# Kernel optimization log

Hardware: AMD Instinct MI355X
Metric: run time of the kernel (lower is better)

The kernel has to match this reference:

```python
import jax, jax.numpy as jnp
import numpy as np

# --- low precision float format: exp=5, man=2, subnormals, nearest-even ---
EXP, MAN = 5, 2
BIAS = 2 ** (EXP - 1) - 1          # 15
EMIN = 1 - BIAS                     # -14 (min normal exponent; clamping here gives subnormals)
MAXV = (2.0 - 2.0 ** (-MAN)) * 2.0 ** BIAS


def _q(x):
    """Round x to nearest FP(exp=5, man=2) value (subnormals, clipped at max)."""
    ax = jnp.abs(x)
    e = jnp.floor(jnp.log2(jnp.where(ax > 0, ax, 1.0)))
    e = jnp.maximum(e, EMIN)
    scale = jnp.exp2(e - MAN)
    q = jnp.round(x / scale) * scale   # jnp.round = half-to-even
    q = jnp.clip(q, -MAXV, MAXV)
    return jnp.where(ax > 0, q, x).astype(x.dtype)


# Quantizer: forward quantize, straight-through (quantized) backward
@jax.custom_vjp
def fq(x):
    return _q(x)

def _fq_fwd(x):
    return _q(x), None

def _fq_bwd(_, g):
    return (_q(g),)

fq.defvjp(_fq_fwd, _fq_bwd)


def conv_valid(x, w):
    return jax.lax.conv_general_dilated(
        x, w, window_strides=(1, 1), padding='VALID',
        dimension_numbers=('NCHW', 'OIHW', 'NCHW'))


def qconv(x, w):
    # QConv2d: input_quant, weight_quant, conv, output_quant
    return fq(conv_valid(fq(x), fq(w)))


def qlinear(x, W, b):
    # QLinear: input_quant, weight_quant (weights + bias), matmul, output_quant
    return fq(fq(x) @ fq(W).T + fq(b))


def batchnorm(x, gamma, beta, eps=1e-5):
    # training-mode BatchNorm2d over (N,H,W) per channel
    m = x.mean(axis=(0, 2, 3), keepdims=True)
    v = x.var(axis=(0, 2, 3), keepdims=True)
    return (x - m) * jax.lax.rsqrt(v + eps) * gamma[None, :, None, None] + beta[None, :, None, None]


def maxpool2(x):
    return jax.lax.reduce_window(x, -jnp.inf, jax.lax.max,
                                 (1, 1, 2, 2), (1, 1, 2, 2), 'VALID')


def setup_inputs() -> dict:
    key = jax.random.key(0)
    ks = jax.random.split(key, 12)
    B = 8192
    inp = {
        'x':   jax.random.normal(ks[0], (B, 1, 32, 32), jnp.float32),
        'w1':  jax.random.normal(ks[1], (6, 1, 5, 5), jnp.float32) * 0.2,
        'g1':  jnp.ones((6,), jnp.float32),
        'be1': jnp.zeros((6,), jnp.float32),
        'w2':  jax.random.normal(ks[2], (16, 6, 5, 5), jnp.float32) * 0.1,
        'g2':  jnp.ones((16,), jnp.float32),
        'be2': jnp.zeros((16,), jnp.float32),
        'fw1': jax.random.normal(ks[3], (120, 400), jnp.float32) * 0.05,
        'fb1': jnp.zeros((120,), jnp.float32),
        'fw2': jax.random.normal(ks[4], (84, 120), jnp.float32) * 0.09,
        'fb2': jnp.zeros((84,), jnp.float32),
        'fw3': jax.random.normal(ks[5], (10, 84), jnp.float32) * 0.1,
        'fb3': jnp.zeros((10,), jnp.float32),
    }
    return inp


def reference(x, w1, g1, be1, w2, g2, be2, fw1, fb1, fw2, fb2, fw3, fb3):
    x = fq(x)                                   # act_error_quant
    x = qconv(x, w1)                            # conv1 (no bias)
    x = batchnorm(x, g1, be1)                   # bn1
    x = fq(x)                                   # act_error_quant
    x = maxpool2(jax.nn.relu(x))                # relu + 2x2 maxpool -> [B,6,14,14]
    x = qconv(x, w2)                            # conv2 -> [B,16,10,10]
    x = batchnorm(x, g2, be2)                   # bn2
    x = fq(x)
    x = maxpool2(jax.nn.relu(x))                # -> [B,16,5,5]
    x = x.reshape(x.shape[0], -1)               # [B,400]
    x = jax.nn.relu(qlinear(x, fw1, fb1))       # fc1
    x = jax.nn.relu(qlinear(x, fw2, fb2))       # fc2
    x = qlinear(x, fw3, fb3)                    # fc3 -> [B,10]
    return x
```

## Files before the change

### kernel.cpp

```cpp
#include <hip/hip_runtime.h>
#include <hip/hip_bf16.h>


#define BATCH 8192

typedef double d4 __attribute__((ext_vector_type(4)));

__device__ __forceinline__ double fq_d(double x) {
    long long b = __double_as_longlong(x);
    long long ab = b & 0x7fffffffffffffffLL;
    if (ab == 0) return x;
    double q;
    if (ab >= 0x3F10000000000000LL) {
        long long r = b + 0x0001FFFFFFFFFFFFLL + ((b >> 50) & 1LL);
        r &= 0xFFFC000000000000LL;
        q = __longlong_as_double(r);
        q = fmin(fmax(q, -57344.0), 57344.0);
    } else {
        q = rint(x * 65536.0) * 1.52587890625e-05;
    }
    return q;
}

__device__ __forceinline__ float fq_f(float x) {
    int b = __float_as_int(x);
    int ab = b & 0x7fffffff;
    if (ab == 0) return x;
    float q;
    if (ab >= 0x38800000) {
        int r = b + 0x000FFFFF + ((b >> 21) & 1);
        r &= 0xFFE00000;
        q = __int_as_float(r);
        q = fminf(fmaxf(q, -57344.0f), 57344.0f);
    } else {
        q = rintf(x * 65536.0f) * 1.52587890625e-05f;
    }
    return q;
}

__device__ __forceinline__ unsigned short bfbits(double q) {
    __hip_bfloat16 h = __float2bfloat16((float)q);
    return *(unsigned short*)&h;
}

__device__ __forceinline__ float bfval(unsigned short u) {
    return __bfloat162float(*(__hip_bfloat16*)&u);
}

__global__ void kprep(const float* __restrict__ w1, const float* __restrict__ w2,
                      const float* __restrict__ fb1, const float* __restrict__ fb2,
                      const float* __restrict__ fb3, const float* __restrict__ fw1,
                      const float* __restrict__ fw2, const float* __restrict__ fw3,
                      float* __restrict__ qw1, float* __restrict__ qw2t,
                      float* __restrict__ qfb1, float* __restrict__ qfb2,
                      float* __restrict__ qfb3, float* __restrict__ Wt1,
                      float* __restrict__ Wt2, float* __restrict__ Wt3) {
    int i = blockIdx.x * 256 + threadIdx.x;
    if (i < 150) { qw1[i] = fq_f(w1[i]); return; }
    i -= 150;
    if (i < 2432) { int k = i >> 4, co = i & 15;
        qw2t[i] = (k < 150) ? fq_f(w2[co * 150 + k]) : 0.0f; return; }
    i -= 2432;
    if (i < 120) { qfb1[i] = fq_f(fb1[i]); return; }
    i -= 120;
    if (i < 84) { qfb2[i] = fq_f(fb2[i]); return; }
    i -= 84;
    if (i < 10) { qfb3[i] = fq_f(fb3[i]); return; }
    i -= 10;
    if (i < 51200) { int k = i / 128, o = i % 128;
        Wt1[i] = (o < 120) ? fq_f(fw1[o * 400 + k]) : 0.0f; return; }
    i -= 51200;
    if (i < 15360) { int k = i / 128, o = i % 128;
        Wt2[i] = (o < 84) ? fq_f(fw2[o * 120 + k]) : 0.0f; return; }
    i -= 15360;
    if (i < 1344) { int k = i / 16, o = i % 16;
        Wt3[i] = (o < 10) ? fq_f(fw3[o * 84 + k]) : 0.0f; return; }
}
#define PREP_TOTAL (150 + 2432 + 120 + 84 + 10 + 51200 + 15360 + 1344)

__global__ __launch_bounds__(512) void kconv1(const float* __restrict__ x,
        const float* __restrict__ qw, const float* __restrict__ g1,
        unsigned short* __restrict__ praw, int nimg_total,
        double* __restrict__ st1) {
    __shared__ float sxf[3 * 1056];
    __shared__ double swd[152];
    __shared__ float sg1[6];
    __shared__ double sred[6][2];
    int t = threadIdx.x;
    int b0 = blockIdx.x * 3;
    int nimg = nimg_total - b0; if (nimg > 3) nimg = 3;
    for (int i = t; i < nimg * 1024; i += 512) {
        int img = i >> 10, idx = i & 1023;
        sxf[img * 1056 + (idx >> 5) * 33 + (idx & 31)] =
            fq_f(x[(size_t)(b0 + img) * 1024 + idx]);
    }
    if (t < 150) swd[t] = (double)qw[t];
    if (t >= 160 && t < 166) sg1[t - 160] = g1[t - 160];
    if (t >= 192 && t < 204) ((double*)sred)[t - 192] = 0.0;
    __syncthreads();
    int ntask = nimg * 168;
    for (int task = t; task < ntask; task += 512) {
        int img = task / 168; int rr = task % 168;
        int co = rr / 28; int rem = rr % 28;
        int ph = rem >> 1;
        int half = rem & 1;
        int i0 = 2 * ph;
        int j0 = half * 14;
        const double* wp = &swd[co * 25];
        double a0[14], a1[14];
        #pragma unroll
        for (int j = 0; j < 14; ++j) { a0[j] = 0.0; a1[j] = 0.0; }
        double wr[5], wq[5];
        #pragma unroll
        for (int u = 0; u < 6; ++u) {
            const float* xr = &sxf[img * 1056 + (i0 + u) * 33 + j0];
            double xv[18];
            #pragma unroll
            for (int k = 0; k < 18; ++k) xv[k] = (double)xr[k];
            if (u < 5) {
                #pragma unroll
                for (int tt = 0; tt < 5; ++tt) wr[tt] = wp[u * 5 + tt];
                #pragma unroll
                for (int j = 0; j < 14; ++j)
                    a0[j] = fma(xv[j], wr[0], fma(xv[j+1], wr[1], fma(xv[j+2], wr[2],
                            fma(xv[j+3], wr[3], fma(xv[j+4], wr[4], a0[j])))));
            }
            if (u >= 1) {
                #pragma unroll
                for (int j = 0; j < 14; ++j)
                    a1[j] = fma(xv[j], wq[0], fma(xv[j+1], wq[1], fma(xv[j+2], wq[2],
                            fma(xv[j+3], wq[3], fma(xv[j+4], wq[4], a1[j])))));
            }
            #pragma unroll
            for (int tt = 0; tt < 5; ++tt) wq[tt] = wr[tt];
        }
        double q0[14], q1[14];
        double s = 0.0, s2 = 0.0;
        #pragma unroll
        for (int j = 0; j < 14; ++j) {
            q0[j] = fq_d(a0[j]); q1[j] = fq_d(a1[j]);
            s += q0[j] + q1[j]; s2 += q0[j] * q0[j] + q1[j] * q1[j];
        }
        bool useMax = (sg1[co] >= 0.0f);
        unsigned short* dst = praw + ((size_t)(b0 + img) * 6 + co) * 196 + ph * 14 + half * 7;
        #pragma unroll
        for (int jp = 0; jp < 7; ++jp) {
            double pmax = fmax(fmax(q0[2*jp], q0[2*jp+1]), fmax(q1[2*jp], q1[2*jp+1]));
            double pmin = fmin(fmin(q0[2*jp], q0[2*jp+1]), fmin(q1[2*jp], q1[2*jp+1]));
            dst[jp] = bfbits(useMax ? pmax : pmin);
        }
        atomicAdd(&sred[co][0], s);
        atomicAdd(&sred[co][1], s2);
    }
    __syncthreads();
    if (t < 12) atomicAdd(&st1[t * 32 + (blockIdx.x & 31)], ((double*)sred)[t]);
}

__global__ void kfinal(const double* __restrict__ st, double* __restrict__ mr,
                       int C, double N) {
    int c = threadIdx.x;
    if (c < C) {
        double s = 0.0, s2 = 0.0;
        for (int b = 0; b < 32; ++b) { s += st[c * 64 + b]; s2 += st[c * 64 + 32 + b]; }
        double m = s / N;
        double v = s2 / N - m * m;
        mr[2 * c] = m;
        mr[2 * c + 1] = 1.0 / sqrt(v + 1e-5);
    }
}

__global__ __launch_bounds__(256) void kbn1(const unsigned short* __restrict__ praw,
        const double* __restrict__ mr1, const float* __restrict__ g1,
        const float* __restrict__ be1, __hip_bfloat16* __restrict__ p1) {
    int idx = blockIdx.x * 256 + threadIdx.x;
    int cb = idx / 49;
    int c = cb % 6;
    int off = (idx % 49) * 4;
    double m = mr1[2 * c], r = mr1[2 * c + 1];
    double gg = (double)g1[c], bb = (double)be1[c];
    ushort4 u = *(const ushort4*)(praw + (size_t)cb * 196 + off);
    ushort4 o;
    double q;
    q = fq_d((((double)bfval(u.x) - m) * r) * gg + bb); o.x = bfbits(fmax(q, 0.0));
    q = fq_d((((double)bfval(u.y) - m) * r) * gg + bb); o.y = bfbits(fmax(q, 0.0));
    q = fq_d((((double)bfval(u.z) - m) * r) * gg + bb); o.z = bfbits(fmax(q, 0.0));
    q = fq_d((((double)bfval(u.w) - m) * r) * gg + bb); o.w = bfbits(fmax(q, 0.0));
    *(ushort4*)((unsigned short*)p1 + (size_t)cb * 196 + off) = o;
}

__global__ __launch_bounds__(512) void kconv2(const __hip_bfloat16* __restrict__ p1,
        const float* __restrict__ qw2t, __hip_bfloat16* __restrict__ c2,
        double* __restrict__ st2) {
    __shared__ float sxf[9408];
    __shared__ float swf[2432];
    __shared__ int soff[152];
    __shared__ unsigned short sep[8][256];
    __shared__ double sred[16][2];
    int t = threadIdx.x;
    int b0 = blockIdx.x * 8;
    const ushort4* srcp = (const ushort4*)(p1 + (size_t)b0 * 1176);
    for (int i = t; i < 2352; i += 512) {
        ushort4 u = srcp[i];
        float* d = &sxf[4 * i];
        d[0] = bfval(u.x);
        d[1] = bfval(u.y);
        d[2] = bfval(u.z);
        d[3] = bfval(u.w);
    }
    {
        const float4* wsrc = (const float4*)qw2t;
        float4* wdst = (float4*)swf;
        for (int i = t; i < 608; i += 512) wdst[i] = wsrc[i];
    }
    if (t < 152)
        soff[t] = (t < 150) ? (t / 25) * 196 + ((t % 25) / 5) * 14 + (t % 5) : 0;
    if (t < 32) ((double*)sred)[t] = 0.0;
    __syncthreads();

    int l = t & 63, w = t >> 6;
    int c = l >> 4, r16 = l & 15;

    d4 pz = {0.0, 0.0, 0.0, 0.0};
    d4 prow = __builtin_amdgcn_mfma_f64_16x16x4f64((double)r16, 0.25, pz, 0, 0, 0);
    d4 pcol = __builtin_amdgcn_mfma_f64_16x16x4f64(1.0, 0.25 * (double)r16, pz, 0, 0, 0);
    int rowidx[4], colidx[4];
    #pragma unroll
    for (int j = 0; j < 4; ++j) { rowidx[j] = (int)prow[j]; colidx[j] = (int)pcol[j]; }

    unsigned short* myep = sep[w];
    double ls = 0.0, ls2 = 0.0;
    int co0 = colidx[0];
    for (int tile = w; tile < 50; tile += 8) {
        int pos = tile * 16 + r16;
        int abase = (pos / 100) * 1176 + ((pos % 100) / 10) * 14 + (pos % 10);
        d4 a0 = {0.0, 0.0, 0.0, 0.0}, a1 = {0.0, 0.0, 0.0, 0.0};
        #pragma unroll
        for (int s = 0; s < 19; ++s) {
            int k0 = 4 * s + c;
            int k1 = 4 * (s + 19) + c;
            double x0 = (double)sxf[abase + soff[k0]];
            double x1 = (double)sxf[abase + soff[k1]];
            double w0 = (double)swf[k0 * 16 + r16];
            double w1 = (double)swf[k1 * 16 + r16];
            a0 = __builtin_amdgcn_mfma_f64_16x16x4f64(x0, w0, a0, 0, 0, 0);
            a1 = __builtin_amdgcn_mfma_f64_16x16x4f64(x1, w1, a1, 0, 0, 0);
        }
        #pragma unroll
        for (int j = 0; j < 4; ++j) {
            double q = fq_d(a0[j] + a1[j]);
            myep[rowidx[j] * 16 + colidx[j]] = bfbits(q);
            ls += q; ls2 += q * q;
        }
        ushort4 v = *(const ushort4*)&myep[l * 4];
        *(ushort4*)((unsigned short*)c2 + ((size_t)b0 * 100 + tile * 16) * 16 + l * 4) = v;
    }
    atomicAdd(&sred[co0][0], ls);
    atomicAdd(&sred[co0][1], ls2);
    __syncthreads();
    if (t < 32) atomicAdd(&st2[t * 32 + (blockIdx.x & 31)], ((double*)sred)[t]);
}

__global__ __launch_bounds__(256) void kfc1(const __hip_bfloat16* __restrict__ c2,
        const double* __restrict__ st2, const float* __restrict__ g2,
        const float* __restrict__ be2, const float* __restrict__ Wt,
        const float* __restrict__ qb, __hip_bfloat16* __restrict__ outb) {
    constexpr int IN = 400, OUT = 120, OUTP = 128, ROWS = 4, BT = 8;
    __shared__ double sx[BT][IN];
    __shared__ double sbn[16][4];
    int t = threadIdx.x;
    int b0 = blockIdx.x * BT;
    if (t < 16) {
        double s = 0.0, s2 = 0.0;
        for (int b = 0; b < 32; ++b) { s += st2[t * 64 + b]; s2 += st2[t * 64 + 32 + b]; }
        double m = s / (819200.0);
        double v = s2 / (819200.0) - m * m;
        sbn[t][0] = m; sbn[t][1] = 1.0 / sqrt(v + 1e-5);
        sbn[t][2] = (double)g2[t]; sbn[t][3] = (double)be2[t];
    }
    __syncthreads();
    for (int i = t; i < BT * IN; i += 256) {
        int cc = i & 15;
        int rem = (i >> 4) % 25;
        int r = i / 400;
        int ph = rem / 5, pw = rem % 5;
        const __hip_bfloat16* src = c2 + ((size_t)(b0 + r) * 100 + 20 * ph + 2 * pw) * 16 + cc;
        double m = sbn[cc][0], rr = sbn[cc][1], gg = sbn[cc][2], bb = sbn[cc][3];
        float f0 = __bfloat162float(src[0]),   f1 = __bfloat162float(src[16]);
        float f2 = __bfloat162float(src[160]), f3 = __bfloat162float(src[176]);
        bool useMax = (rr * gg) >= 0.0;
        float v = useMax ? fmaxf(fmaxf(f0, f1), fmaxf(f2, f3))
                         : fminf(fminf(f0, f1), fminf(f2, f3));
        double q = fq_d((((double)v - m) * rr) * gg + bb);
        sx[r][cc * 25 + rem] = fmax(q, 0.0);
    }
    __syncthreads();
    int o = t % OUTP;
    int g = t / OUTP;
    double acc[ROWS];
    double bias = (o < OUT) ? (double)qb[o] : 0.0;
    #pragma unroll
    for (int r = 0; r < ROWS; ++r) acc[r] = bias;
    #pragma unroll 4
    for (int k = 0; k < IN; ++k) {
        double w = (double)Wt[k * OUTP + o];
        #pragma unroll
        for (int r = 0; r < ROWS; ++r)
            acc[r] = fma(sx[g * ROWS + r][k], w, acc[r]);
    }
    if (o < OUT) {
        #pragma unroll
        for (int r = 0; r < ROWS; ++r) {
            double q = fq_d(acc[r]);
            if (q < 0.0) q = 0.0;
            outb[(size_t)(b0 + g * ROWS + r) * OUT + o] = __float2bfloat16((float)q);
        }
    }
}

__global__ __launch_bounds__(256) void kfc23(const __hip_bfloat16* __restrict__ a1,
        const float* __restrict__ Wt2, const float* __restrict__ qfb2,
        const float* __restrict__ Wt3, const float* __restrict__ qfb3,
        float* __restrict__ out) {
    __shared__ double sx1[16][120];
    __shared__ double s2[16][84];
    int t = threadIdx.x;
    int b0 = blockIdx.x * 16;
    for (int i = t; i < 16 * 120; i += 256) {
        int r = i / 120, k = i % 120;
        sx1[r][k] = (double)__bfloat162float(a1[(size_t)(b0 + r) * 120 + k]);
    }
    __syncthreads();
    {
        int o = t % 128, g = t / 128;
        double acc[8];
        double bias = (o < 84) ? (double)qfb2[o] : 0.0;
        #pragma unroll
        for (int r = 0; r < 8; ++r) acc[r] = bias;
        #pragma unroll 4
        for (int k = 0; k < 120; ++k) {
            double w = (double)Wt2[k * 128 + o];
            #pragma unroll
            for (int r = 0; r < 8; ++r)
                acc[r] = fma(sx1[g * 8 + r][k], w, acc[r]);
        }
        if (o < 84) {
            #pragma unroll
            for (int r = 0; r < 8; ++r) {
                double q = fq_d(acc[r]);
                s2[g * 8 + r][o] = fmax(q, 0.0);
            }
        }
    }
    __syncthreads();
    {
        int o = t % 16, g = t / 16;
        double acc = (o < 10) ? (double)qfb3[o] : 0.0;
        #pragma unroll 4
        for (int k = 0; k < 84; ++k)
            acc = fma(s2[g][k], (double)Wt3[k * 16 + o], acc);
        if (o < 10)
            out[(size_t)(b0 + g) * 10 + o] = (float)fq_d(acc);
    }
}

extern "C" void kernel_launch(void* const* d_in, const int* in_sizes, int n_in,
                              void* d_out, int out_size, void* d_ws, size_t ws_size,
                              hipStream_t stream) {
    const float* x   = (const float*)d_in[0];
    const float* w1  = (const float*)d_in[1];
    const float* g1  = (const float*)d_in[2];
    const float* be1 = (const float*)d_in[3];
    const float* w2  = (const float*)d_in[4];
    const float* g2  = (const float*)d_in[5];
    const float* be2 = (const float*)d_in[6];
    const float* fw1 = (const float*)d_in[7];
    const float* fb1 = (const float*)d_in[8];
    const float* fw2 = (const float*)d_in[9];
    const float* fb2 = (const float*)d_in[10];
    const float* fw3 = (const float*)d_in[11];
    const float* fb3 = (const float*)d_in[12];

    char* ws = (char*)d_ws;
    double* stats1 = (double*)(ws + 0);
    double* stats2 = (double*)(ws + 3072);
    double* mr1    = (double*)(ws + 11264);
    float* qw1  = (float*)(ws + 12288);
    float* qw2t = (float*)(ws + 13312);
    float* qfb1 = (float*)(ws + 23040);
    float* qfb2 = (float*)(ws + 23552);
    float* qfb3 = (float*)(ws + 24064);
    float* Wt1  = (float*)(ws + 24576);
    float* Wt2  = (float*)(ws + 229376);
    float* Wt3  = (float*)(ws + 290816);
    unsigned short* praw = (unsigned short*)(ws + 303104);
    __hip_bfloat16* p1 = (__hip_bfloat16*)(ws + 77373440);
    __hip_bfloat16* c2 = (__hip_bfloat16*)(ws + 303104);
    __hip_bfloat16* a1 = (__hip_bfloat16*)(ws + 303104 + 26214400);

    hipMemsetAsync(ws, 0, 11264, stream);

    kprep<<<(PREP_TOTAL + 255) / 256, 256, 0, stream>>>(
        w1, w2, fb1, fb2, fb3, fw1, fw2, fw3,
        qw1, qw2t, qfb1, qfb2, qfb3, Wt1, Wt2, Wt3);

    kconv1<<<(BATCH + 2) / 3, 512, 0, stream>>>(x, qw1, g1, praw, BATCH, stats1);
    kfinal<<<1, 32, 0, stream>>>(stats1, mr1, 6, (double)BATCH * 784.0);
    kbn1<<<BATCH * 6 * 49 / 256, 256, 0, stream>>>(praw, mr1, g1, be1, p1);
    kconv2<<<BATCH / 8, 512, 0, stream>>>(p1, qw2t, c2, stats2);
    kfc1<<<BATCH / 8, 256, 0, stream>>>(c2, stats2, g2, be2, Wt1, qfb1, a1);
    kfc23<<<BATCH / 16, 256, 0, stream>>>(a1, Wt2, qfb2, Wt3, qfb3, (float*)d_out);
}
```

Measured before the change: 378.3 us.

## Fuse BN1 finalize and normalize into conv2 load; split conv2 MFMA accumulators four ways

Removes the kfinal and kbn1 kernels. Each conv2 block now computes the BN1 mean and rstd from the partial stats and applies normalize, quantize and ReLU while loading the pooled conv1 output into shared memory. This drops one full intermediate write and read of the [B,6,14,14] tensor and two launches, at the cost of recomputing the stats per block. The conv2 MFMA chain also uses four independent accumulators instead of two, to shorten the dependency chains.

```diff
diff --git a/kernel.cpp b/kernel.cpp
--- a/kernel.cpp
+++ b/kernel.cpp
@@ -156,57 +156,18 @@
     if (t < 12) atomicAdd(&st1[t * 32 + (blockIdx.x & 31)], ((double*)sred)[t]);
 }
 
-__global__ void kfinal(const double* __restrict__ st, double* __restrict__ mr,
-                       int C, double N) {
-    int c = threadIdx.x;
-    if (c < C) {
-        double s = 0.0, s2 = 0.0;
-        for (int b = 0; b < 32; ++b) { s += st[c * 64 + b]; s2 += st[c * 64 + 32 + b]; }
-        double m = s / N;
-        double v = s2 / N - m * m;
-        mr[2 * c] = m;
-        mr[2 * c + 1] = 1.0 / sqrt(v + 1e-5);
-    }
-}
-
-__global__ __launch_bounds__(256) void kbn1(const unsigned short* __restrict__ praw,
-        const double* __restrict__ mr1, const float* __restrict__ g1,
-        const float* __restrict__ be1, __hip_bfloat16* __restrict__ p1) {
-    int idx = blockIdx.x * 256 + threadIdx.x;
-    int cb = idx / 49;
-    int c = cb % 6;
-    int off = (idx % 49) * 4;
-    double m = mr1[2 * c], r = mr1[2 * c + 1];
-    double gg = (double)g1[c], bb = (double)be1[c];
-    ushort4 u = *(const ushort4*)(praw + (size_t)cb * 196 + off);
-    ushort4 o;
-    double q;
-    q = fq_d((((double)bfval(u.x) - m) * r) * gg + bb); o.x = bfbits(fmax(q, 0.0));
-    q = fq_d((((double)bfval(u.y) - m) * r) * gg + bb); o.y = bfbits(fmax(q, 0.0));
-    q = fq_d((((double)bfval(u.z) - m) * r) * gg + bb); o.z = bfbits(fmax(q, 0.0));
-    q = fq_d((((double)bfval(u.w) - m) * r) * gg + bb); o.w = bfbits(fmax(q, 0.0));
-    *(ushort4*)((unsigned short*)p1 + (size_t)cb * 196 + off) = o;
-}
-
-__global__ __launch_bounds__(512) void kconv2(const __hip_bfloat16* __restrict__ p1,
-        const float* __restrict__ qw2t, __hip_bfloat16* __restrict__ c2,
-        double* __restrict__ st2) {
+__global__ __launch_bounds__(512) void kconv2(const unsigned short* __restrict__ praw,
+        const double* __restrict__ st1, const float* __restrict__ g1,
+        const float* __restrict__ be1, const float* __restrict__ qw2t,
+        __hip_bfloat16* __restrict__ c2, double* __restrict__ st2) {
     __shared__ float sxf[9408];
     __shared__ float swf[2432];
     __shared__ int soff[152];
     __shared__ unsigned short sep[8][256];
     __shared__ double sred[16][2];
+    __shared__ double sbn1[6][4];
     int t = threadIdx.x;
     int b0 = blockIdx.x * 8;
-    const ushort4* srcp = (const ushort4*)(p1 + (size_t)b0 * 1176);
-    for (int i = t; i < 2352; i += 512) {
-        ushort4 u = srcp[i];
-        float* d = &sxf[4 * i];
-        d[0] = bfval(u.x);
-        d[1] = bfval(u.y);
-        d[2] = bfval(u.z);
-        d[3] = bfval(u.w);
-    }
     {
         const float4* wsrc = (const float4*)qw2t;
         float4* wdst = (float4*)swf;
@@ -215,6 +176,28 @@
     if (t < 152)
         soff[t] = (t < 150) ? (t / 25) * 196 + ((t % 25) / 5) * 14 + (t % 5) : 0;
     if (t < 32) ((double*)sred)[t] = 0.0;
+    if (t < 6) {
+        double s = 0.0, s2 = 0.0;
+        for (int b = 0; b < 32; ++b) { s += st1[t * 64 + b]; s2 += st1[t * 64 + 32 + b]; }
+        double m = s / 6422528.0;
+        double v = s2 / 6422528.0 - m * m;
+        sbn1[t][0] = m; sbn1[t][1] = 1.0 / sqrt(v + 1e-5);
+        sbn1[t][2] = (double)g1[t]; sbn1[t][3] = (double)be1[t];
+    }
+    __syncthreads();
+    const ushort4* srcp = (const ushort4*)(praw + (size_t)b0 * 1176);
+    for (int i = t; i < 2352; i += 512) {
+        ushort4 u = srcp[i];
+        int ch = ((4 * i) % 1176) / 196;
+        double m = sbn1[ch][0], r = sbn1[ch][1];
+        double gg = sbn1[ch][2], bb = sbn1[ch][3];
+        float* d = &sxf[4 * i];
+        double q;
+        q = fq_d((((double)bfval(u.x) - m) * r) * gg + bb); d[0] = (float)fmax(q, 0.0);
+        q = fq_d((((double)bfval(u.y) - m) * r) * gg + bb); d[1] = (float)fmax(q, 0.0);
+        q = fq_d((((double)bfval(u.z) - m) * r) * gg + bb); d[2] = (float)fmax(q, 0.0);
+        q = fq_d((((double)bfval(u.w) - m) * r) * gg + bb); d[3] = (float)fmax(q, 0.0);
+    }
     __syncthreads();
 
     int l = t & 63, w = t >> 6;
@@ -234,20 +217,31 @@
         int pos = tile * 16 + r16;
         int abase = (pos / 100) * 1176 + ((pos % 100) / 10) * 14 + (pos % 10);
         d4 a0 = {0.0, 0.0, 0.0, 0.0}, a1 = {0.0, 0.0, 0.0, 0.0};
-        #pragma unroll
-        for (int s = 0; s < 19; ++s) {
+        d4 a2 = {0.0, 0.0, 0.0, 0.0}, a3 = {0.0, 0.0, 0.0, 0.0};
+        #pragma unroll
+        for (int s = 0; s < 10; ++s) {
             int k0 = 4 * s + c;
-            int k1 = 4 * (s + 19) + c;
+            int k1 = 4 * (s + 10) + c;
             double x0 = (double)sxf[abase + soff[k0]];
+            double w0 = (double)swf[k0 * 16 + r16];
+            a0 = __builtin_amdgcn_mfma_f64_16x16x4f64(x0, w0, a0, 0, 0, 0);
             double x1 = (double)sxf[abase + soff[k1]];
-            double w0 = (double)swf[k0 * 16 + r16];
             double w1 = (double)swf[k1 * 16 + r16];
-            a0 = __builtin_amdgcn_mfma_f64_16x16x4f64(x0, w0, a0, 0, 0, 0);
             a1 = __builtin_amdgcn_mfma_f64_16x16x4f64(x1, w1, a1, 0, 0, 0);
+            if (s < 9) {
+                int k2 = 4 * (s + 20) + c;
+                int k3 = 4 * (s + 29) + c;
+                double x2 = (double)sxf[abase + soff[k2]];
+                double w2 = (double)swf[k2 * 16 + r16];
+                a2 = __builtin_amdgcn_mfma_f64_16x16x4f64(x2, w2, a2, 0, 0, 0);
+                double x3 = (double)sxf[abase + soff[k3]];
+                double w3 = (double)swf[k3 * 16 + r16];
+                a3 = __builtin_amdgcn_mfma_f64_16x16x4f64(x3, w3, a3, 0, 0, 0);
+            }
         }
         #pragma unroll
         for (int j = 0; j < 4; ++j) {
-            double q = fq_d(a0[j] + a1[j]);
+            double q = fq_d((a0[j] + a1[j]) + (a2[j] + a3[j]));
             myep[rowidx[j] * 16 + colidx[j]] = bfbits(q);
             ls += q; ls2 += q * q;
         }
@@ -383,7 +377,6 @@
     char* ws = (char*)d_ws;
     double* stats1 = (double*)(ws + 0);
     double* stats2 = (double*)(ws + 3072);
-    double* mr1    = (double*)(ws + 11264);
     float* qw1  = (float*)(ws + 12288);
     float* qw2t = (float*)(ws + 13312);
     float* qfb1 = (float*)(ws + 23040);
@@ -393,9 +386,8 @@
     float* Wt2  = (float*)(ws + 229376);
     float* Wt3  = (float*)(ws + 290816);
     unsigned short* praw = (unsigned short*)(ws + 303104);
-    __hip_bfloat16* p1 = (__hip_bfloat16*)(ws + 77373440);
-    __hip_bfloat16* c2 = (__hip_bfloat16*)(ws + 303104);
-    __hip_bfloat16* a1 = (__hip_bfloat16*)(ws + 303104 + 26214400);
+    __hip_bfloat16* c2 = (__hip_bfloat16*)(ws + 19570688);
+    __hip_bfloat16* a1 = (__hip_bfloat16*)(ws + 45785088);
 
     hipMemsetAsync(ws, 0, 11264, stream);
 
@@ -404,9 +396,7 @@
         qw1, qw2t, qfb1, qfb2, qfb3, Wt1, Wt2, Wt3);
 
     kconv1<<<(BATCH + 2) / 3, 512, 0, stream>>>(x, qw1, g1, praw, BATCH, stats1);
-    kfinal<<<1, 32, 0, stream>>>(stats1, mr1, 6, (double)BATCH * 784.0);
-    kbn1<<<BATCH * 6 * 49 / 256, 256, 0, stream>>>(praw, mr1, g1, be1, p1);
-    kconv2<<<BATCH / 8, 512, 0, stream>>>(p1, qw2t, c2, stats2);
+    kconv2<<<BATCH / 8, 512, 0, stream>>>(praw, stats1, g1, be1, qw2t, c2, stats2);
     kfc1<<<BATCH / 8, 256, 0, stream>>>(c2, stats2, g2, be2, Wt1, qfb1, a1);
     kfc23<<<BATCH / 16, 256, 0, stream>>>(a1, Wt2, qfb2, Wt3, qfb3, (float*)d_out);
 }
```

Result: no change. 373.6 us (-1.3%).
